# Kernel tuning notes

Hardware: AMD Instinct MI355X
Metric: run time of the kernel (lower is better)

Reference implementation:

```python
import jax, jax.numpy as jnp
import numpy as np

N, E, C, Z, B, L = 50000, 800000, 32, 4, 8, 2
DEG = 16.0  # avg num neighbors = E / N


def ssp(x):
    # ShiftedSoftPlus
    return jax.nn.softplus(x) - jnp.log(2.0).astype(x.dtype)


def setup_inputs() -> dict:
    key = jax.random.key(0)
    ks = jax.random.split(key, 13)
    f32 = jnp.float32
    return {
        "node_features": jax.random.normal(ks[0], (N, 4 * C), f32),
        "node_attrs": jax.random.uniform(ks[1], (N, Z), f32),
        "edge_index": jax.random.randint(ks[2], (2, E), 0, N),
        "edge_embedding": jax.random.uniform(ks[3], (E, B), f32),
        "edge_attrs": jax.random.normal(ks[4], (E, 4), f32),
        "W0": jax.random.normal(ks[5], (L, C, C), f32) / np.sqrt(C),
        "W1": jax.random.normal(ks[6], (L, C, C), f32) / np.sqrt(C),
        "Wr1": jax.random.normal(ks[7], (L, B, B), f32) / np.sqrt(B),
        "Wr2": jax.random.normal(ks[8], (L, B, 5 * C), f32) / np.sqrt(B),
        "Ws": jax.random.normal(ks[9], (L, C, 2 * C), f32) / np.sqrt(C),
        "Wv": jax.random.normal(ks[10], (L, C, C), f32) / np.sqrt(C),
        "Wsc_s": jax.random.normal(ks[11], (L, C, Z, 2 * C), f32) / np.sqrt(C * Z),
        "Wsc_v": jax.random.normal(ks[12], (L, C, Z, C), f32) / np.sqrt(C * Z),
    }


def reference(node_features, node_attrs, edge_index, edge_embedding, edge_attrs,
              W0, W1, Wr1, Wr2, Ws, Wv, Wsc_s, Wsc_v):
    src, dst = edge_index[0], edge_index[1]
    Y0 = edge_attrs[:, :1]            # [E,1]  l=0 sph harmonic
    Yv = edge_attrs[:, 1:]            # [E,3]  l=1 sph harmonic
    x = node_features
    for l in range(L):
        s_in = x[:, :C]                          # [N,C]   scalars
        v_in = x[:, C:].reshape(N, C, 3)         # [N,C,3] vectors
        # linear (channel mixing per irrep)
        s = s_in @ W0[l]
        v = jnp.einsum('nci,cf->nfi', v_in, W1[l])
        # gather source node features per edge
        se = s[src]                              # [E,C]
        ve = v[src]                              # [E,C,3]
        # radial MLP -> per-edge tensor-product path weights (5 paths)
        w = jax.nn.silu(edge_embedding @ Wr1[l]) @ Wr2[l]   # [E,5C]
        w1, w2, w3, w4, w5 = jnp.split(w, 5, axis=-1)
        # tensor-product messages
        m_s = w1 * se * Y0 + w4 * jnp.einsum('eci,ei->ec', ve, Yv)          # 0ex0e->0e, 1ex1e->0e
        m_v = (w2[..., None] * se[..., None] * Yv[:, None, :]               # 0ex1e->1e
               + w3[..., None] * ve * Y0[..., None]                         # 1ex0e->1e
               + w5[..., None] * jnp.cross(ve, Yv[:, None, :]))             # 1ex1e->1e
        # scatter-sum to destination nodes, normalize by avg degree
        agg_s = jax.ops.segment_sum(m_s, dst, num_segments=N) / DEG
        agg_v = jax.ops.segment_sum(m_v, dst, num_segments=N) / DEG
        # output linear: scalars -> C feature scalars + C gates, vectors -> C
        out_s = agg_s @ Ws[l]                                               # [N,2C]
        out_v = jnp.einsum('nci,cf->nfi', agg_v, Wv[l])                     # [N,C,3]
        # self-connection (FullyConnectedTensorProduct with node_attrs)
        out_s = out_s + jnp.einsum('nc,nz,czf->nf', s_in, node_attrs, Wsc_s[l])
        out_v = out_v + jnp.einsum('nci,nz,czf->nfi', v_in, node_attrs, Wsc_v[l])
        # equivariant Gate nonlinearity
        feat = ssp(out_s[:, :C])
        gates = ssp(out_s[:, C:])
        gv = out_v * gates[..., None]
        new_x = jnp.concatenate([feat, gv.reshape(N, 3 * C)], axis=-1)
        x = x + new_x  # resnet (irreps match across layers)
    return x
```

## Files before the change

### kernel.cpp

```cpp
#include <hip/hip_runtime.h>
#include <math.h>

#define NN 50000
#define NE 800000
#define Cc 32
#define Zz 4
#define Bb 8
#define NL 2
#define DEG_INV (1.0f/16.0f)
#define SCAN_PAD 53248
#define SCAN_BLOCKS 49
#define EBLK (NE / 256)
#define NBLK (NN / 8)


__device__ __forceinline__ float ssp_f(float x) {
    float sp = fmaxf(x, 0.0f) + log1pf(expf(-fabsf(x)));
    return sp - 0.69314718055994530942f;
}
__device__ __forceinline__ float silu_f(float x) {
    return x / (1.0f + expf(-x));
}
__device__ __forceinline__ unsigned bf16rn(float f) {
    unsigned u = __float_as_uint(f);
    return (u + 0x7fffu + ((u >> 16) & 1u)) >> 16;
}


__global__ void hist_kernel(const int* __restrict__ ei, int* __restrict__ counts) {
    int e = blockIdx.x * 256 + threadIdx.x;
    if (e < NE) atomicAdd(&counts[ei[NE + e]], 1);
}

__global__ void scan_part_kernel(const int* __restrict__ counts,
                                 int* __restrict__ blocksum) {
    __shared__ int red[256];
    int b = blockIdx.x, t = threadIdx.x;
    int4 v = ((const int4*)counts)[b * 256 + t];
    red[t] = v.x + v.y + v.z + v.w;
    __syncthreads();
    for (int off = 128; off > 0; off >>= 1) {
        if (t < off) red[t] += red[t + off];
        __syncthreads();
    }
    if (t == 0) blocksum[b] = red[0];
}

__global__ void scan_top_kernel(int* __restrict__ blocksum,
                                int* __restrict__ base) {
    int lane = threadIdx.x;
    int v = (lane < SCAN_BLOCKS) ? blocksum[lane] : 0;
    int inc = v;
    #pragma unroll
    for (int off = 1; off < 64; off <<= 1) {
        int n = __shfl_up(inc, off, 64);
        if (lane >= off) inc += n;
    }
    if (lane < SCAN_BLOCKS) blocksum[lane] = inc - v;
    if (lane == 0) base[NN] = NE;
}

__global__ void scan_fin_kernel(const int* __restrict__ counts,
                                const int* __restrict__ blockoff,
                                int* __restrict__ base,
                                int* __restrict__ cursor) {
    __shared__ int wsum[4];
    int b = blockIdx.x, t = threadIdx.x;
    int4 v = ((const int4*)counts)[b * 256 + t];
    int s = v.x + v.y + v.z + v.w;
    int lane = t & 63, wid = t >> 6;
    int inc = s;
    #pragma unroll
    for (int off = 1; off < 64; off <<= 1) {
        int n = __shfl_up(inc, off, 64);
        if (lane >= off) inc += n;
    }
    if (lane == 63) wsum[wid] = inc;
    __syncthreads();
    int add = blockoff[b];
    for (int w = 0; w < wid; ++w) add += wsum[w];
    int e0 = inc - s + add;
    int e1 = e0 + v.x;
    int e2 = e1 + v.y;
    int e3 = e2 + v.z;
    int idx = b * 1024 + t * 4;
    if (idx + 0 < NN) { base[idx + 0] = e0; cursor[idx + 0] = e0; }
    if (idx + 1 < NN) { base[idx + 1] = e1; cursor[idx + 1] = e1; }
    if (idx + 2 < NN) { base[idx + 2] = e2; cursor[idx + 2] = e2; }
    if (idx + 3 < NN) { base[idx + 3] = e3; cursor[idx + 3] = e3; }
}

__global__ void prep_kernel(const int* __restrict__ ei,
                            const float* __restrict__ emb,
                            const float* __restrict__ eattr,
                            const float* __restrict__ Wr1,
                            int* __restrict__ cursor,
                            uint4* __restrict__ rec,
                            const float* __restrict__ nf,
                            const float* __restrict__ W0,
                            const float* __restrict__ W1,
                            float* __restrict__ x,
                            unsigned* __restrict__ svb) {
    __shared__ float wr1s[128];
    __shared__ float xs[8][128];
    int t = threadIdx.x;
    int b = blockIdx.x;
    if (b < EBLK) {
        if (t < 128) wr1s[t] = Wr1[t];
        __syncthreads();
        int e = b * 256 + t;
        int src = ei[e];
        int dst = ei[NE + e];
        int pos = atomicAdd(&cursor[dst], 1);

        const float4* s4 = (const float4*)emb + (size_t)e * 2;
        float4 a = s4[0], bb = s4[1];
        float em[8] = {a.x, a.y, a.z, a.w, bb.x, bb.y, bb.z, bb.w};
        float h0[8], h1[8];
        #pragma unroll
        for (int j = 0; j < 8; ++j) {
            float acc0 = 0.f, acc1 = 0.f;
            #pragma unroll
            for (int k = 0; k < 8; ++k) {
                acc0 = fmaf(em[k], wr1s[k * 8 + j], acc0);
                acc1 = fmaf(em[k], wr1s[64 + k * 8 + j], acc1);
            }
            h0[j] = silu_f(acc0);
            h1[j] = silu_f(acc1);
        }
        uint4 u0, u1;
        u0.x = bf16rn(h0[0]) | (bf16rn(h0[1]) << 16);
        u0.y = bf16rn(h0[2]) | (bf16rn(h0[3]) << 16);
        u0.z = bf16rn(h0[4]) | (bf16rn(h0[5]) << 16);
        u0.w = bf16rn(h0[6]) | (bf16rn(h0[7]) << 16);
        u1.x = bf16rn(h1[0]) | (bf16rn(h1[1]) << 16);
        u1.y = bf16rn(h1[2]) | (bf16rn(h1[3]) << 16);
        u1.z = bf16rn(h1[4]) | (bf16rn(h1[5]) << 16);
        u1.w = bf16rn(h1[6]) | (bf16rn(h1[7]) << 16);
        uint4* r = rec + (size_t)pos * 4;
        r[0] = u0;
        r[1] = u1;
        r[2] = ((const uint4*)eattr)[e];
        r[3] = make_uint4((unsigned)src, 0u, 0u, 0u);
    } else {
        int node0 = (b - EBLK) * 8;
        #pragma unroll
        for (int k = 0; k < 4; ++k) {
            int idx = t + k * 256;
            int n = idx >> 7, col = idx & 127;
            float val = nf[(size_t)(node0 + n) * 128 + col];
            xs[n][col] = val;
            x[(size_t)(node0 + n) * 128 + col] = val;
        }
        __syncthreads();
        int n = t >> 5, f = t & 31;
        int gn = node0 + n;
        float acc_s = 0.f, a0 = 0.f, a1 = 0.f, a2 = 0.f;
        #pragma unroll
        for (int c = 0; c < Cc; ++c) {
            float w0 = W0[c * Cc + f];
            float w1 = W1[c * Cc + f];
            acc_s = fmaf(xs[n][c], w0, acc_s);
            a0 = fmaf(xs[n][32 + c * 3 + 0], w1, a0);
            a1 = fmaf(xs[n][32 + c * 3 + 1], w1, a1);
            a2 = fmaf(xs[n][32 + c * 3 + 2], w1, a2);
        }
        unsigned* o = svb + (size_t)gn * 64;
        o[f]      = bf16rn(acc_s) | (bf16rn(a0) << 16);
        o[32 + f] = bf16rn(a1)    | (bf16rn(a2) << 16);
    }
}

#define PROC_EDGE_PK(ua, Yv, se, v0, v1, v2)                                 \
    do {                                                                     \
        float hh0 = __uint_as_float(ua.x << 16);                             \
        float hh1 = __uint_as_float(ua.x & 0xffff0000u);                     \
        float hh2 = __uint_as_float(ua.y << 16);                             \
        float hh3 = __uint_as_float(ua.y & 0xffff0000u);                     \
        float hh4 = __uint_as_float(ua.z << 16);                             \
        float hh5 = __uint_as_float(ua.z & 0xffff0000u);                     \
        float hh6 = __uint_as_float(ua.w << 16);                             \
        float hh7 = __uint_as_float(ua.w & 0xffff0000u);                     \
        float w1 = 0.f, w2 = 0.f, w3 = 0.f, w4 = 0.f, w5 = 0.f;              \
        w1 = fmaf(hh0, wr2s[0][c], w1); w2 = fmaf(hh0, wr2s[0][32 + c], w2); \
        w3 = fmaf(hh0, wr2s[0][64 + c], w3); w4 = fmaf(hh0, wr2s[0][96 + c], w4); \
        w5 = fmaf(hh0, wr2s[0][128 + c], w5);                                \
        w1 = fmaf(hh1, wr2s[1][c], w1); w2 = fmaf(hh1, wr2s[1][32 + c], w2); \
        w3 = fmaf(hh1, wr2s[1][64 + c], w3); w4 = fmaf(hh1, wr2s[1][96 + c], w4); \
        w5 = fmaf(hh1, wr2s[1][128 + c], w5);                                \
        w1 = fmaf(hh2, wr2s[2][c], w1); w2 = fmaf(hh2, wr2s[2][32 + c], w2); \
        w3 = fmaf(hh2, wr2s[2][64 + c], w3); w4 = fmaf(hh2, wr2s[2][96 + c], w4); \
        w5 = fmaf(hh2, wr2s[2][128 + c], w5);                                \
        w1 = fmaf(hh3, wr2s[3][c], w1); w2 = fmaf(hh3, wr2s[3][32 + c], w2); \
        w3 = fmaf(hh3, wr2s[3][64 + c], w3); w4 = fmaf(hh3, wr2s[3][96 + c], w4); \
        w5 = fmaf(hh3, wr2s[3][128 + c], w5);                                \
        w1 = fmaf(hh4, wr2s[4][c], w1); w2 = fmaf(hh4, wr2s[4][32 + c], w2); \
        w3 = fmaf(hh4, wr2s[4][64 + c], w3); w4 = fmaf(hh4, wr2s[4][96 + c], w4); \
        w5 = fmaf(hh4, wr2s[4][128 + c], w5);                                \
        w1 = fmaf(hh5, wr2s[5][c], w1); w2 = fmaf(hh5, wr2s[5][32 + c], w2); \
        w3 = fmaf(hh5, wr2s[5][64 + c], w3); w4 = fmaf(hh5, wr2s[5][96 + c], w4); \
        w5 = fmaf(hh5, wr2s[5][128 + c], w5);                                \
        w1 = fmaf(hh6, wr2s[6][c], w1); w2 = fmaf(hh6, wr2s[6][32 + c], w2); \
        w3 = fmaf(hh6, wr2s[6][64 + c], w3); w4 = fmaf(hh6, wr2s[6][96 + c], w4); \
        w5 = fmaf(hh6, wr2s[6][128 + c], w5);                                \
        w1 = fmaf(hh7, wr2s[7][c], w1); w2 = fmaf(hh7, wr2s[7][32 + c], w2); \
        w3 = fmaf(hh7, wr2s[7][64 + c], w3); w4 = fmaf(hh7, wr2s[7][96 + c], w4); \
        w5 = fmaf(hh7, wr2s[7][128 + c], w5);                                \
        float dot = v0 * Yv.y + v1 * Yv.z + v2 * Yv.w;                       \
        ms += w1 * se * Yv.x + w4 * dot;                                     \
        float cx = v1 * Yv.w - v2 * Yv.z;                                    \
        float cy = v2 * Yv.y - v0 * Yv.w;                                    \
        float cz = v0 * Yv.z - v1 * Yv.y;                                    \
        mv0 += w2 * se * Yv.y + w3 * v0 * Yv.x + w5 * cx;                    \
        mv1 += w2 * se * Yv.z + w3 * v1 * Yv.x + w5 * cy;                    \
        mv2 += w2 * se * Yv.w + w3 * v2 * Yv.x + w5 * cz;                    \
    } while (0)

#define UNPACK_SV(p, se, v0, v1, v2)                                         \
    unsigned ulo_##se = (p)[c], uhi_##se = (p)[32 + c];                      \
    float se = __uint_as_float(ulo_##se << 16);                              \
    float v0 = __uint_as_float(ulo_##se & 0xffff0000u);                      \
    float v1 = __uint_as_float(uhi_##se << 16);                              \
    float v2 = __uint_as_float(uhi_##se & 0xffff0000u)

__global__ void agg_kernel(const int* __restrict__ base,
                           const uint4* __restrict__ rec,
                           const int lsel,
                           const unsigned* __restrict__ svb,
                           const float* __restrict__ Wr2,
                           float* __restrict__ agg) {
    __shared__ float wr2s[8][160];
    int t = threadIdx.x;
    for (int i = t; i < 8 * 160; i += 256) ((float*)wr2s)[i] = Wr2[i];
    __syncthreads();
    int n = blockIdx.x * 4 + (t >> 6);
    int lane = t & 63;
    int half = lane >> 5;
    int c = lane & 31;
    int jb = base[n], je = base[n + 1];
    float ms = 0.f, mv0 = 0.f, mv1 = 0.f, mv2 = 0.f;

    int j = jb + half;
    for (; j + 2 < je; j += 4) {
        const uint4* r0 = rec + (size_t)j * 4;
        const uint4* r1 = rec + (size_t)(j + 2) * 4;
        uint4 u0 = r0[lsel];
        uint4 u1 = r1[lsel];
        float4 Y0 = *(const float4*)(r0 + 2);
        float4 Y1 = *(const float4*)(r1 + 2);
        int s0 = (int)r0[3].x;
        int s1 = (int)r1[3].x;
        const unsigned* p0 = svb + (size_t)s0 * 64;
        const unsigned* p1 = svb + (size_t)s1 * 64;
        UNPACK_SV(p0, seA, vA0, vA1, vA2);
        UNPACK_SV(p1, seB, vB0, vB1, vB2);
        PROC_EDGE_PK(u0, Y0, seA, vA0, vA1, vA2);
        PROC_EDGE_PK(u1, Y1, seB, vB0, vB1, vB2);
    }
    if (j < je) {
        const uint4* r0 = rec + (size_t)j * 4;
        uint4 u0 = r0[lsel];
        float4 Y0 = *(const float4*)(r0 + 2);
        int s0 = (int)r0[3].x;
        const unsigned* p0 = svb + (size_t)s0 * 64;
        UNPACK_SV(p0, seA, vA0, vA1, vA2);
        PROC_EDGE_PK(u0, Y0, seA, vA0, vA1, vA2);
    }

    ms  += __shfl_xor(ms, 32, 64);
    mv0 += __shfl_xor(mv0, 32, 64);
    mv1 += __shfl_xor(mv1, 32, 64);
    mv2 += __shfl_xor(mv2, 32, 64);

    if (half == 0) {
        float* ap = agg + (size_t)n * 128;
        ap[c]      = ms * DEG_INV;
        ap[32 + c] = mv0 * DEG_INV;
        ap[64 + c] = mv1 * DEG_INV;
        ap[96 + c] = mv2 * DEG_INV;
    }
}

template <int WANT_SV>
__global__ void post_pre_kernel(float* __restrict__ x,
                                const float* __restrict__ attrs,
                                const float* __restrict__ agg,
                                const float* __restrict__ Ws,
                                const float* __restrict__ Wv,
                                const float* __restrict__ Wsc_s,
                                const float* __restrict__ Wsc_v,
                                const float* __restrict__ W0n,
                                const float* __restrict__ W1n,
                                unsigned* __restrict__ svb) {
    __shared__ float shx[16][128];
    __shared__ float sha[16][128];
    int t = threadIdx.x;
    int node0 = blockIdx.x * 16;
    #pragma unroll
    for (int k = 0; k < 4; ++k) {
        int f4 = t + k * 128;
        int n = f4 >> 5, col4 = f4 & 31;
        int gn = node0 + n;
        if (gn < NN) {
            ((float4*)&shx[n][0])[col4] = ((const float4*)(x + (size_t)gn * 128))[col4];
            ((float4*)&sha[n][0])[col4] = ((const float4*)(agg + (size_t)gn * 128))[col4];
        }
    }
    __syncthreads();
    int g = t >> 5, f = t & 31;

    float az[4][4];
    #pragma unroll
    for (int k = 0; k < 4; ++k) {
        int gn = node0 + g + k * 4;
        if (gn < NN) {
            float4 a4 = ((const float4*)attrs)[gn];
            az[k][0] = a4.x; az[k][1] = a4.y; az[k][2] = a4.z; az[k][3] = a4.w;
        } else {
            az[k][0] = az[k][1] = az[k][2] = az[k][3] = 0.f;
        }
    }

    float os0[4] = {0, 0, 0, 0}, os1[4] = {0, 0, 0, 0};
    float ov0[4] = {0, 0, 0, 0}, ov1[4] = {0, 0, 0, 0}, ov2[4] = {0, 0, 0, 0};

    #pragma unroll 2
    for (int c = 0; c < Cc; ++c) {
        float ws0 = Ws[c * 64 + f];
        float ws1 = Ws[c * 64 + 32 + f];
        float wv  = Wv[c * 32 + f];
        #pragma unroll
        for (int k = 0; k < 4; ++k) {
            int n = g + k * 4;
            float as  = sha[n][c];
            float av0 = sha[n][32 + c];
            float av1 = sha[n][64 + c];
            float av2 = sha[n][96 + c];
            os0[k] = fmaf(as, ws0, os0[k]);
            os1[k] = fmaf(as, ws1, os1[k]);
            ov0[k] = fmaf(av0, wv, ov0[k]);
            ov1[k] = fmaf(av1, wv, ov1[k]);
            ov2[k] = fmaf(av2, wv, ov2[k]);
        }
        #pragma unroll
        for (int z = 0; z < 4; ++z) {
            int cz = c * 4 + z;
            float wss0 = Wsc_s[cz * 64 + f];
            float wss1 = Wsc_s[cz * 64 + 32 + f];
            float wsv  = Wsc_v[cz * 32 + f];
            #pragma unroll
            for (int k = 0; k < 4; ++k) {
                int n = g + k * 4;
                float azv = az[k][z];
                float sa = shx[n][c] * azv;
                os0[k] = fmaf(sa, wss0, os0[k]);
                os1[k] = fmaf(sa, wss1, os1[k]);
                float va = azv * wsv;
                ov0[k] = fmaf(shx[n][32 + c * 3 + 0], va, ov0[k]);
                ov1[k] = fmaf(shx[n][32 + c * 3 + 1], va, ov1[k]);
                ov2[k] = fmaf(shx[n][32 + c * 3 + 2], va, ov2[k]);
            }
        }
    }

    float ns[4], nv0[4], nv1[4], nv2[4];
    #pragma unroll
    for (int k = 0; k < 4; ++k) {
        int n = g + k * 4;
        int gn = node0 + n;
        float feat = ssp_f(os0[k]);
        float gate = ssp_f(os1[k]);
        ns[k]  = shx[n][f] + feat;
        nv0[k] = shx[n][32 + f * 3 + 0] + ov0[k] * gate;
        nv1[k] = shx[n][32 + f * 3 + 1] + ov1[k] * gate;
        nv2[k] = shx[n][32 + f * 3 + 2] + ov2[k] * gate;
        if (gn < NN) {
            float* xp = x + (size_t)gn * 128;
            xp[f] = ns[k];
            xp[32 + f * 3 + 0] = nv0[k];
            xp[32 + f * 3 + 1] = nv1[k];
            xp[32 + f * 3 + 2] = nv2[k];
        }
    }

    if (WANT_SV) {
        __syncthreads();
        #pragma unroll
        for (int k = 0; k < 4; ++k) {
            int n = g + k * 4;
            sha[n][f] = ns[k];
            sha[n][32 + f * 3 + 0] = nv0[k];
            sha[n][32 + f * 3 + 1] = nv1[k];
            sha[n][32 + f * 3 + 2] = nv2[k];
        }
        __syncthreads();
        float bs[4] = {0, 0, 0, 0};
        float b0[4] = {0, 0, 0, 0}, b1[4] = {0, 0, 0, 0}, b2[4] = {0, 0, 0, 0};
        #pragma unroll 4
        for (int c = 0; c < Cc; ++c) {
            float w0 = W0n[c * Cc + f];
            float w1 = W1n[c * Cc + f];
            #pragma unroll
            for (int k = 0; k < 4; ++k) {
                int n = g + k * 4;
                bs[k] = fmaf(sha[n][c], w0, bs[k]);
                b0[k] = fmaf(sha[n][32 + c * 3 + 0], w1, b0[k]);
                b1[k] = fmaf(sha[n][32 + c * 3 + 1], w1, b1[k]);
                b2[k] = fmaf(sha[n][32 + c * 3 + 2], w1, b2[k]);
            }
        }
        #pragma unroll
        for (int k = 0; k < 4; ++k) {
            int gn = node0 + g + k * 4;
            if (gn < NN) {
                unsigned* o = svb + (size_t)gn * 64;
                o[f]      = bf16rn(bs[k]) | (bf16rn(b0[k]) << 16);
                o[32 + f] = bf16rn(b1[k]) | (bf16rn(b2[k]) << 16);
            }
        }
    }
}

__global__ void edge_atomic_kernel(const int* __restrict__ ei,
                                   const float* __restrict__ emb,
                                   const float* __restrict__ eattr,
                                   const unsigned* __restrict__ svb,
                                   const float* __restrict__ Wr1,
                                   const float* __restrict__ Wr2,
                                   float* __restrict__ agg) {
    int t = threadIdx.x;
    int eg = t >> 5;
    int c = t & 31;
    int e = blockIdx.x * 8 + eg;
    if (e >= NE) return;
    int src = ei[e];
    int dst = ei[NE + e];
    float h = 0.f;
    if (c < 8) {
        #pragma unroll
        for (int k = 0; k < 8; ++k)
            h = fmaf(emb[e * 8 + k], Wr1[k * 8 + c], h);
        h = silu_f(h);
    }
    float w1 = 0.f, w2 = 0.f, w3 = 0.f, w4 = 0.f, w5 = 0.f;
    #pragma unroll
    for (int j = 0; j < 8; ++j) {
        float hj = __shfl(h, j, 32);
        const float* wr = Wr2 + j * 160;
        w1 = fmaf(hj, wr[c], w1);
        w2 = fmaf(hj, wr[32 + c], w2);
        w3 = fmaf(hj, wr[64 + c], w3);
        w4 = fmaf(hj, wr[96 + c], w4);
        w5 = fmaf(hj, wr[128 + c], w5);
    }
    float Y0  = eattr[e * 4 + 0];
    float Yv0 = eattr[e * 4 + 1];
    float Yv1 = eattr[e * 4 + 2];
    float Yv2 = eattr[e * 4 + 3];
    const unsigned* p = svb + (size_t)src * 64;
    unsigned ulo = p[c], uhi = p[32 + c];
    float se  = __uint_as_float(ulo << 16);
    float ve0 = __uint_as_float(ulo & 0xffff0000u);
    float ve1 = __uint_as_float(uhi << 16);
    float ve2 = __uint_as_float(uhi & 0xffff0000u);
    float dot = ve0 * Yv0 + ve1 * Yv1 + ve2 * Yv2;
    float msg = (w1 * se * Y0 + w4 * dot) * DEG_INV;
    float cx = ve1 * Yv2 - ve2 * Yv1;
    float cy = ve2 * Yv0 - ve0 * Yv2;
    float cz = ve0 * Yv1 - ve1 * Yv0;
    float mv0 = (w2 * se * Yv0 + w3 * ve0 * Y0 + w5 * cx) * DEG_INV;
    float mv1 = (w2 * se * Yv1 + w3 * ve1 * Y0 + w5 * cy) * DEG_INV;
    float mv2 = (w2 * se * Yv2 + w3 * ve2 * Y0 + w5 * cz) * DEG_INV;
    float* ap = agg + (size_t)dst * 128;
    atomicAdd(&ap[c], msg);
    atomicAdd(&ap[32 + c], mv0);
    atomicAdd(&ap[64 + c], mv1);
    atomicAdd(&ap[96 + c], mv2);
}

__global__ void init_kernel(const float* __restrict__ nf,
                            const float* __restrict__ W0,
                            const float* __restrict__ W1,
                            float* __restrict__ x,
                            unsigned* __restrict__ svb) {
    __shared__ float xs[8][128];
    int t = threadIdx.x;
    int node0 = blockIdx.x * 8;
    #pragma unroll
    for (int k = 0; k < 4; ++k) {
        int idx = t + k * 256;
        int n = idx >> 7, col = idx & 127;
        float val = nf[(size_t)(node0 + n) * 128 + col];
        xs[n][col] = val;
        x[(size_t)(node0 + n) * 128 + col] = val;
    }
    __syncthreads();
    int n = t >> 5, f = t & 31;
    int gn = node0 + n;
    float acc_s = 0.f, a0 = 0.f, a1 = 0.f, a2 = 0.f;
    #pragma unroll
    for (int c = 0; c < Cc; ++c) {
        float w0 = W0[c * Cc + f];
        float w1 = W1[c * Cc + f];
        acc_s = fmaf(xs[n][c], w0, acc_s);
        a0 = fmaf(xs[n][32 + c * 3 + 0], w1, a0);
        a1 = fmaf(xs[n][32 + c * 3 + 1], w1, a1);
        a2 = fmaf(xs[n][32 + c * 3 + 2], w1, a2);
    }
    unsigned* o = svb + (size_t)gn * 64;
    o[f]      = bf16rn(acc_s) | (bf16rn(a0) << 16);
    o[32 + f] = bf16rn(a1)    | (bf16rn(a2) << 16);
}

extern "C" void kernel_launch(void* const* d_in, const int* in_sizes, int n_in,
                              void* d_out, int out_size, void* d_ws, size_t ws_size,
                              hipStream_t stream) {
    const float* node_features  = (const float*)d_in[0];
    const float* node_attrs     = (const float*)d_in[1];
    const int*   edge_index     = (const int*)d_in[2];
    const float* edge_embedding = (const float*)d_in[3];
    const float* edge_attrs     = (const float*)d_in[4];
    const float* W0    = (const float*)d_in[5];
    const float* W1    = (const float*)d_in[6];
    const float* Wr1   = (const float*)d_in[7];
    const float* Wr2   = (const float*)d_in[8];
    const float* Ws    = (const float*)d_in[9];
    const float* Wv    = (const float*)d_in[10];
    const float* Wsc_s = (const float*)d_in[11];
    const float* Wsc_v = (const float*)d_in[12];

    float* x = (float*)d_out;

    float* ws = (float*)d_ws;
    unsigned* svb = (unsigned*)ws;
    float* agg  = (float*)(svb + (size_t)NN * 64);
    uint4* rec  = (uint4*)(agg + (size_t)NN * 128);
    int* counts   = (int*)(rec + (size_t)NE * 4);
    int* base     = counts + SCAN_PAD;
    int* cursor   = base + NN + 1;
    int* blocksum = cursor + NN;
    size_t needed = ((char*)(blocksum + SCAN_BLOCKS)) - (char*)d_ws;

    bool use_sorted = ws_size >= needed;
    const int PP_GRID = (NN + 15) / 16;
    const int AGG_GRID = (NN + 3) / 4;

    if (use_sorted) {
        hipMemsetAsync(counts, 0, SCAN_PAD * sizeof(int), stream);
        hist_kernel<<<NE / 256, 256, 0, stream>>>(edge_index, counts);
        scan_part_kernel<<<SCAN_BLOCKS, 256, 0, stream>>>(counts, blocksum);
        scan_top_kernel<<<1, 64, 0, stream>>>(blocksum, base);
        scan_fin_kernel<<<SCAN_BLOCKS, 256, 0, stream>>>(counts, blocksum,
                                                         base, cursor);
        prep_kernel<<<EBLK + NBLK, 256, 0, stream>>>(
            edge_index, edge_embedding, edge_attrs, Wr1,
            cursor, rec,
            node_features, W0, W1, x, svb);

        agg_kernel<<<AGG_GRID, 256, 0, stream>>>(base, rec, 0, svb, Wr2, agg);
        post_pre_kernel<1><<<PP_GRID, 128, 0, stream>>>(
            x, node_attrs, agg, Ws, Wv, Wsc_s, Wsc_v,
            W0 + Cc * Cc, W1 + Cc * Cc, svb);
        agg_kernel<<<AGG_GRID, 256, 0, stream>>>(base, rec, 1, svb,
                                                 Wr2 + Bb * 5 * Cc, agg);
        post_pre_kernel<0><<<PP_GRID, 128, 0, stream>>>(
            x, node_attrs, agg,
            Ws + Cc * 2 * Cc, Wv + Cc * Cc,
            Wsc_s + Cc * Zz * 2 * Cc, Wsc_v + Cc * Zz * Cc,
            nullptr, nullptr, nullptr);
    } else {
        hipMemcpyAsync(x, node_features, (size_t)NN * 128 * sizeof(float),
                       hipMemcpyDeviceToDevice, stream);
        for (int l = 0; l < NL; ++l) {
            hipMemsetAsync(agg, 0, (size_t)NN * 128 * sizeof(float), stream);
            init_kernel<<<NN / 8, 256, 0, stream>>>(
                x, W0 + l * Cc * Cc, W1 + l * Cc * Cc, x, svb);
            edge_atomic_kernel<<<NE / 8, 256, 0, stream>>>(
                edge_index, edge_embedding, edge_attrs, svb,
                Wr1 + l * Bb * Bb, Wr2 + l * Bb * 5 * Cc, agg);
            post_pre_kernel<0><<<PP_GRID, 128, 0, stream>>>(
                x, node_attrs, agg,
                Ws + l * Cc * 2 * Cc, Wv + l * Cc * Cc,
                Wsc_s + l * Cc * Zz * 2 * Cc, Wsc_v + l * Cc * Zz * Cc,
                nullptr, nullptr, nullptr);
        }
    }
}
```

Measured before the change: 483.0 us.

## Shrink edge records to 48 bytes and map one node per half-wave

Edge attributes are now stored as bf16 alongside the source index, so each sorted edge record takes three uint4s instead of four. This cuts the record bytes written in prep and read twice in aggregation. The aggregation kernel also changes from 64 lanes splitting a node's edges in two halves with a shuffle reduction to 32 lanes per node, 8 nodes per block, walking edges two at a time. Rounding Y to bf16 adds precision error, and the new mapping changes per-node load balance and memory-level parallelism.

```diff
diff --git a/kernel.cpp b/kernel.cpp
--- a/kernel.cpp
+++ b/kernel.cpp
@@ -25,6 +25,8 @@
     unsigned u = __float_as_uint(f);
     return (u + 0x7fffu + ((u >> 16) & 1u)) >> 16;
 }
+#define BLO(u) __uint_as_float((u) << 16)
+#define BHI(u) __uint_as_float((u) & 0xffff0000u)
 
 
 __global__ void hist_kernel(const int* __restrict__ ei, int* __restrict__ counts) {
@@ -137,11 +139,16 @@
         u1.y = bf16rn(h1[2]) | (bf16rn(h1[3]) << 16);
         u1.z = bf16rn(h1[4]) | (bf16rn(h1[5]) << 16);
         u1.w = bf16rn(h1[6]) | (bf16rn(h1[7]) << 16);
-        uint4* r = rec + (size_t)pos * 4;
+        float4 Yf = ((const float4*)eattr)[e];
+        uint4 m;
+        m.x = bf16rn(Yf.x) | (bf16rn(Yf.y) << 16);
+        m.y = bf16rn(Yf.z) | (bf16rn(Yf.w) << 16);
+        m.z = (unsigned)src;
+        m.w = 0u;
+        uint4* r = rec + (size_t)pos * 3;
         r[0] = u0;
         r[1] = u1;
-        r[2] = ((const uint4*)eattr)[e];
-        r[3] = make_uint4((unsigned)src, 0u, 0u, 0u);
+        r[2] = m;
     } else {
         int node0 = (b - EBLK) * 8;
         #pragma unroll
@@ -173,14 +180,10 @@
 
 #define PROC_EDGE_PK(ua, Yv, se, v0, v1, v2)                                 \
     do {                                                                     \
-        float hh0 = __uint_as_float(ua.x << 16);                             \
-        float hh1 = __uint_as_float(ua.x & 0xffff0000u);                     \
-        float hh2 = __uint_as_float(ua.y << 16);                             \
-        float hh3 = __uint_as_float(ua.y & 0xffff0000u);                     \
-        float hh4 = __uint_as_float(ua.z << 16);                             \
-        float hh5 = __uint_as_float(ua.z & 0xffff0000u);                     \
-        float hh6 = __uint_as_float(ua.w << 16);                             \
-        float hh7 = __uint_as_float(ua.w & 0xffff0000u);                     \
+        float hh0 = BLO(ua.x), hh1 = BHI(ua.x);                              \
+        float hh2 = BLO(ua.y), hh3 = BHI(ua.y);                              \
+        float hh4 = BLO(ua.z), hh5 = BHI(ua.z);                              \
+        float hh6 = BLO(ua.w), hh7 = BHI(ua.w);                              \
         float w1 = 0.f, w2 = 0.f, w3 = 0.f, w4 = 0.f, w5 = 0.f;              \
         w1 = fmaf(hh0, wr2s[0][c], w1); w2 = fmaf(hh0, wr2s[0][32 + c], w2); \
         w3 = fmaf(hh0, wr2s[0][64 + c], w3); w4 = fmaf(hh0, wr2s[0][96 + c], w4); \
@@ -218,10 +221,10 @@
 
 #define UNPACK_SV(p, se, v0, v1, v2)                                         \
     unsigned ulo_##se = (p)[c], uhi_##se = (p)[32 + c];                      \
-    float se = __uint_as_float(ulo_##se << 16);                              \
-    float v0 = __uint_as_float(ulo_##se & 0xffff0000u);                      \
-    float v1 = __uint_as_float(uhi_##se << 16);                              \
-    float v2 = __uint_as_float(uhi_##se & 0xffff0000u)
+    float se = BLO(ulo_##se);                                                \
+    float v0 = BHI(ulo_##se);                                                \
+    float v1 = BLO(uhi_##se);                                                \
+    float v2 = BHI(uhi_##se)
 
 __global__ void agg_kernel(const int* __restrict__ base,
                            const uint4* __restrict__ rec,
@@ -233,52 +236,46 @@
     int t = threadIdx.x;
     for (int i = t; i < 8 * 160; i += 256) ((float*)wr2s)[i] = Wr2[i];
     __syncthreads();
-    int n = blockIdx.x * 4 + (t >> 6);
-    int lane = t & 63;
-    int half = lane >> 5;
-    int c = lane & 31;
+    int n = blockIdx.x * 8 + (t >> 5);
+    int c = t & 31;
     int jb = base[n], je = base[n + 1];
     float ms = 0.f, mv0 = 0.f, mv1 = 0.f, mv2 = 0.f;
 
-    int j = jb + half;
-    for (; j + 2 < je; j += 4) {
-        const uint4* r0 = rec + (size_t)j * 4;
-        const uint4* r1 = rec + (size_t)(j + 2) * 4;
+    int j = jb;
+    for (; j + 1 < je; j += 2) {
+        const uint4* r0 = rec + (size_t)j * 3;
+        const uint4* r1 = r0 + 3;
         uint4 u0 = r0[lsel];
+        uint4 m0 = r0[2];
         uint4 u1 = r1[lsel];
-        float4 Y0 = *(const float4*)(r0 + 2);
-        float4 Y1 = *(const float4*)(r1 + 2);
-        int s0 = (int)r0[3].x;
-        int s1 = (int)r1[3].x;
+        uint4 m1 = r1[2];
+        int s0 = (int)m0.z;
+        int s1 = (int)m1.z;
         const unsigned* p0 = svb + (size_t)s0 * 64;
         const unsigned* p1 = svb + (size_t)s1 * 64;
         UNPACK_SV(p0, seA, vA0, vA1, vA2);
         UNPACK_SV(p1, seB, vB0, vB1, vB2);
+        float4 Y0 = make_float4(BLO(m0.x), BHI(m0.x), BLO(m0.y), BHI(m0.y));
+        float4 Y1 = make_float4(BLO(m1.x), BHI(m1.x), BLO(m1.y), BHI(m1.y));
         PROC_EDGE_PK(u0, Y0, seA, vA0, vA1, vA2);
         PROC_EDGE_PK(u1, Y1, seB, vB0, vB1, vB2);
     }
     if (j < je) {
-        const uint4* r0 = rec + (size_t)j * 4;
+        const uint4* r0 = rec + (size_t)j * 3;
         uint4 u0 = r0[lsel];
-        float4 Y0 = *(const float4*)(r0 + 2);
-        int s0 = (int)r0[3].x;
+        uint4 m0 = r0[2];
+        int s0 = (int)m0.z;
         const unsigned* p0 = svb + (size_t)s0 * 64;
         UNPACK_SV(p0, seA, vA0, vA1, vA2);
+        float4 Y0 = make_float4(BLO(m0.x), BHI(m0.x), BLO(m0.y), BHI(m0.y));
         PROC_EDGE_PK(u0, Y0, seA, vA0, vA1, vA2);
     }
 
-    ms  += __shfl_xor(ms, 32, 64);
-    mv0 += __shfl_xor(mv0, 32, 64);
-    mv1 += __shfl_xor(mv1, 32, 64);
-    mv2 += __shfl_xor(mv2, 32, 64);
-
-    if (half == 0) {
-        float* ap = agg + (size_t)n * 128;
-        ap[c]      = ms * DEG_INV;
-        ap[32 + c] = mv0 * DEG_INV;
-        ap[64 + c] = mv1 * DEG_INV;
-        ap[96 + c] = mv2 * DEG_INV;
-    }
+    float* ap = agg + (size_t)n * 128;
+    ap[c]      = ms * DEG_INV;
+    ap[32 + c] = mv0 * DEG_INV;
+    ap[64 + c] = mv1 * DEG_INV;
+    ap[96 + c] = mv2 * DEG_INV;
 }
 
 template <int WANT_SV>
@@ -459,10 +456,10 @@
     float Yv2 = eattr[e * 4 + 3];
     const unsigned* p = svb + (size_t)src * 64;
     unsigned ulo = p[c], uhi = p[32 + c];
-    float se  = __uint_as_float(ulo << 16);
-    float ve0 = __uint_as_float(ulo & 0xffff0000u);
-    float ve1 = __uint_as_float(uhi << 16);
-    float ve2 = __uint_as_float(uhi & 0xffff0000u);
+    float se  = BLO(ulo);
+    float ve0 = BHI(ulo);
+    float ve1 = BLO(uhi);
+    float ve2 = BHI(uhi);
     float dot = ve0 * Yv0 + ve1 * Yv1 + ve2 * Yv2;
     float msg = (w1 * se * Y0 + w4 * dot) * DEG_INV;
     float cx = ve1 * Yv2 - ve2 * Yv1;
@@ -535,7 +532,7 @@
     unsigned* svb = (unsigned*)ws;
     float* agg  = (float*)(svb + (size_t)NN * 64);
     uint4* rec  = (uint4*)(agg + (size_t)NN * 128);
-    int* counts   = (int*)(rec + (size_t)NE * 4);
+    int* counts   = (int*)(rec + (size_t)NE * 3);
     int* base     = counts + SCAN_PAD;
     int* cursor   = base + NN + 1;
     int* blocksum = cursor + NN;
@@ -543,7 +540,6 @@
 
     bool use_sorted = ws_size >= needed;
     const int PP_GRID = (NN + 15) / 16;
-    const int AGG_GRID = (NN + 3) / 4;
 
     if (use_sorted) {
         hipMemsetAsync(counts, 0, SCAN_PAD * sizeof(int), stream);
@@ -557,12 +553,12 @@
             cursor, rec,
             node_features, W0, W1, x, svb);
 
-        agg_kernel<<<AGG_GRID, 256, 0, stream>>>(base, rec, 0, svb, Wr2, agg);
+        agg_kernel<<<NN / 8, 256, 0, stream>>>(base, rec, 0, svb, Wr2, agg);
         post_pre_kernel<1><<<PP_GRID, 128, 0, stream>>>(
             x, node_attrs, agg, Ws, Wv, Wsc_s, Wsc_v,
             W0 + Cc * Cc, W1 + Cc * Cc, svb);
-        agg_kernel<<<AGG_GRID, 256, 0, stream>>>(base, rec, 1, svb,
-                                                 Wr2 + Bb * 5 * Cc, agg);
+        agg_kernel<<<NN / 8, 256, 0, stream>>>(base, rec, 1, svb,
+                                               Wr2 + Bb * 5 * Cc, agg);
         post_pre_kernel<0><<<PP_GRID, 128, 0, stream>>>(
             x, node_attrs, agg,
             Ws + Cc * 2 * Cc, Wv + Cc * Cc,
```

After: 464.6 us. 1.04x faster.
